# Optimization experiments

Measured on AMD Instinct MI355X. Metric: run time of the kernel, lower is better.

Reference implementation:

```python
import jax, jax.numpy as jnp
import numpy as np

# config constants
H = 2048          # hidden_size
I_MOE = 1408      # moe_intermediate_size
E = 8             # n_routed_experts
TOP_K = 2         # num_experts_per_tok
NG = 4            # n_group
TOPK_G = 2        # topk_group
SCALE = 2.5       # routed_scaling_factor
N_SHARED = 2      # n_shared_experts
I_SHARED = I_MOE * N_SHARED
B, S = 1, 2048


def setup_inputs() -> dict:
    key = jax.random.key(0)
    ks = jax.random.split(key, 9)
    sc = 0.02
    return {
        "x": jax.random.normal(ks[0], (B, S, H), dtype=jnp.float32),
        "router_weight": jax.random.normal(ks[1], (E, H), dtype=jnp.float32) * sc,
        "e_score_correction_bias": jnp.zeros((E,), dtype=jnp.float32),
        "gate_w": jax.random.normal(ks[2], (E, I_MOE, H), dtype=jnp.float32) * sc,
        "up_w": jax.random.normal(ks[3], (E, I_MOE, H), dtype=jnp.float32) * sc,
        "down_w": jax.random.normal(ks[4], (E, H, I_MOE), dtype=jnp.float32) * sc,
        "shared_gate_w": jax.random.normal(ks[5], (I_SHARED, H), dtype=jnp.float32) * sc,
        "shared_up_w": jax.random.normal(ks[6], (I_SHARED, H), dtype=jnp.float32) * sc,
        "shared_down_w": jax.random.normal(ks[7], (H, I_SHARED), dtype=jnp.float32) * sc,
    }


def _mlp(x, gw, uw, dw):
    # SwiGLU MLP: down( silu(gate(x)) * up(x) )
    return (jax.nn.silu(x @ gw.T) * (x @ uw.T)) @ dw.T


def _route(x2d, rw, bias):
    T = x2d.shape[0]
    logits = x2d.astype(jnp.float32) @ rw.astype(jnp.float32).T          # [T,E]
    scores = jax.nn.sigmoid(logits)                                       # [T,E]
    sfc = scores + bias[None, :]                                          # [T,E]
    # group scores: sum of top-2 per group
    grp = sfc.reshape(T, NG, E // NG)
    group_scores = jnp.sum(jax.lax.top_k(grp, 2)[0], axis=-1)             # [T,NG]
    grp_idx = jax.lax.top_k(group_scores, TOPK_G)[1]                      # [T,topk_group]
    group_mask = jnp.zeros((T, NG), jnp.float32).at[
        jnp.arange(T)[:, None], grp_idx].set(1.0)                         # [T,NG]
    score_mask = jnp.repeat(group_mask, E // NG, axis=1)                  # [T,E]
    masked = jnp.where(score_mask > 0, sfc, 0.0)
    topk_idx = jax.lax.top_k(masked, TOP_K)[1]                            # [T,K]
    topk_w = jnp.take_along_axis(scores, topk_idx, axis=1)                # [T,K]
    topk_w = topk_w / (jnp.sum(topk_w, axis=-1, keepdims=True) + 1e-20)   # norm_topk_prob
    return topk_idx, topk_w * SCALE


def reference(x, router_weight, e_score_correction_bias, gate_w, up_w, down_w,
              shared_gate_w, shared_up_w, shared_down_w):
    orig_shape = x.shape
    x2d = x.reshape(-1, H)                                                # [T,H]
    T = x2d.shape[0]
    topk_idx, topk_w = _route(x2d, router_weight, e_score_correction_bias)
    # per-token per-expert combine weights [T,E] (top-k indices are distinct per token)
    cw = jnp.zeros((T, E), jnp.float32).at[
        jnp.arange(T)[:, None], topk_idx].add(topk_w)

    def expert_body(acc, ws):
        gw, uw, dw, cwe = ws  # gw/uw:[I,H], dw:[H,I], cwe:[T]
        y = _mlp(x2d, gw, uw, dw)
        return acc + cwe[:, None] * y, None

    routed, _ = jax.lax.scan(expert_body, jnp.zeros_like(x2d),
                             (gate_w, up_w, down_w, cw.T))
    out = routed.reshape(orig_shape) + _mlp(x, shared_gate_w, shared_up_w, shared_down_w)
    return out
```

## Files before the change

kernel.cpp:

```cpp
#include <hip/hip_runtime.h>
#include <hip/hip_bf16.h>
#include <math.h>

#define H 2048
#define IMOE 1408
#define NEXP 8
#define T_TOK 2048
#define ISH 2816
#define SCALEF 2.5f

#define NT_GU_R (IMOE / 64)
#define NT_GU_S (ISH / 64)
#define NT_DN   (H / 128)
#define GU_GRID (39 * NT_GU_R + 16 * NT_GU_S)
#define DN_GRID (39 * NT_DN + 16 * NT_DN)

typedef __attribute__((ext_vector_type(8))) short short8;
typedef __attribute__((ext_vector_type(4))) short short4v;
typedef __attribute__((ext_vector_type(4))) float floatx4;

union U8 { short8 s; unsigned u[4]; };

__device__ inline float b2f(short v) {
    unsigned int u = ((unsigned int)(unsigned short)v) << 16;
    float f; __builtin_memcpy(&f, &u, 4); return f;
}
__device__ inline short f2b(float f) {
    __hip_bfloat16 h = __float2bfloat16(f);
    short s; __builtin_memcpy(&s, &h, 2); return s;
}
__device__ __forceinline__ unsigned pkbf16(float a, float b) {
    float2 t; t.x = a; t.y = b;
    __hip_bfloat162 h2 = __float22bfloat162_rn(t);
    unsigned u; __builtin_memcpy(&u, &h2, 4); return u;
}

__device__ __forceinline__ void async16(const short* g, short* l) {
    __builtin_amdgcn_global_load_lds(
        (const __attribute__((address_space(1))) unsigned*)g,
        (__attribute__((address_space(3))) unsigned*)l, 16, 0, 0);
}

__device__ __forceinline__ int xcd_map(int orig, int nwg) {
    int q = nwg >> 3, r = nwg & 7;
    int x = orig & 7, s = orig >> 3;
    int base = (x < r) ? x * (q + 1) : r * (q + 1) + (x - r) * q;
    return base + s;
}

__global__ __launch_bounds__(256) void router_kernel(
    const float* __restrict__ x, const float* __restrict__ rw,
    const float* __restrict__ bias,
    int* __restrict__ cnt, int* __restrict__ tokList, int* __restrict__ slotList,
    float* __restrict__ pairW)
{
    const int wid  = (blockIdx.x * 256 + threadIdx.x) >> 6;
    const int lane = threadIdx.x & 63;
    if (wid >= T_TOK) return;
    const float* xr = x + (size_t)wid * H;

    float acc[NEXP];
#pragma unroll
    for (int e = 0; e < NEXP; ++e) acc[e] = 0.f;

#pragma unroll
    for (int c = 0; c < 8; ++c) {
        int idx = (c * 64 + lane) * 4;
        floatx4 xv = *(const floatx4*)(xr + idx);
#pragma unroll
        for (int e = 0; e < NEXP; ++e) {
            floatx4 wv = *(const floatx4*)(rw + e * H + idx);
            acc[e] += xv.x * wv.x + xv.y * wv.y + xv.z * wv.z + xv.w * wv.w;
        }
    }
#pragma unroll
    for (int e = 0; e < NEXP; ++e)
        for (int off = 32; off; off >>= 1)
            acc[e] += __shfl_xor(acc[e], off, 64);

    if (lane == 0) {
        float s[NEXP], sfc[NEXP];
#pragma unroll
        for (int e = 0; e < NEXP; ++e) {
            s[e]   = 1.0f / (1.0f + expf(-acc[e]));
            sfc[e] = s[e] + bias[e];
        }
        float gs[4];
#pragma unroll
        for (int g = 0; g < 4; ++g) gs[g] = sfc[2 * g] + sfc[2 * g + 1];
        int g1 = 0;
        for (int g = 1; g < 4; ++g) if (gs[g] > gs[g1]) g1 = g;
        int g2 = -1;
        for (int g = 0; g < 4; ++g) {
            if (g == g1) continue;
            if (g2 < 0 || gs[g] > gs[g2]) g2 = g;
        }
        float msk[NEXP];
#pragma unroll
        for (int e = 0; e < NEXP; ++e) {
            int g = e >> 1;
            msk[e] = (g == g1 || g == g2) ? sfc[e] : 0.0f;
        }
        int e1 = 0;
        for (int e = 1; e < NEXP; ++e) if (msk[e] > msk[e1]) e1 = e;
        int e2 = -1;
        for (int e = 0; e < NEXP; ++e) {
            if (e == e1) continue;
            if (e2 < 0 || msk[e] > msk[e2]) e2 = e;
        }
        float w1 = s[e1], w2 = s[e2];
        float inv = SCALEF / (w1 + w2 + 1e-20f);
        w1 *= inv; w2 *= inv;
        int p1 = atomicAdd(&cnt[e1], 1);
        tokList[e1 * T_TOK + p1]  = wid;
        slotList[e1 * T_TOK + p1] = 2 * wid;
        pairW[2 * wid] = w1;
        int p2 = atomicAdd(&cnt[e2], 1);
        tokList[e2 * T_TOK + p2]  = wid;
        slotList[e2 * T_TOK + p2] = 2 * wid + 1;
        pairW[2 * wid + 1] = w2;
    }
}

__global__ void plan_kernel(const int* __restrict__ cnt, int* __restrict__ meta)
{
    if (blockIdx.x != 0 || threadIdx.x != 0) return;
    int base = 0, gu = 0, dn = 0;
    meta[20] = 0; meta[32] = 0;
    for (int e = 0; e < NEXP; ++e) {
        int M = cnt[e];
        meta[e] = M;
        meta[9 + e] = base;
        base += M;
        int MT = (M + 127) >> 7;
        gu += MT * NT_GU_R;
        dn += MT * NT_DN;
        meta[21 + e] = gu;
        meta[33 + e] = dn;
    }
    meta[8]  = T_TOK;
    meta[17] = 0;
    meta[29] = gu + 16 * NT_GU_S;
    meta[41] = dn + 16 * NT_DN;
}

__global__ __launch_bounds__(256) void convert_kernel(
    const float* __restrict__ src, short* __restrict__ dst, int n4)
{
    int idx = blockIdx.x * 256 + threadIdx.x;
    int stride = gridDim.x * 256;
    for (; idx < n4; idx += stride) {
        floatx4 v = *(const floatx4*)(src + (size_t)idx * 4);
        short4v o = { f2b(v.x), f2b(v.y), f2b(v.z), f2b(v.w) };
        *(short4v*)(dst + (size_t)idx * 4) = o;
    }
}

__global__ __launch_bounds__(256) void gu_gemm(
    const short* __restrict__ xb,
    const float* __restrict__ gw, const float* __restrict__ uw,
    const float* __restrict__ sgw, const float* __restrict__ suw,
    short* __restrict__ hiddenP, short* __restrict__ hiddenS,
    const int* __restrict__ tokList, const int* __restrict__ meta)
{
    const int total = meta[29];
    if (blockIdx.x >= total) return;
    const int idx = xcd_map(blockIdx.x, total);
    int e = 0;
    while (e < 8 && idx >= meta[21 + e]) ++e;

    int M, NT, Nout, rowBase;
    const float *b1, *b2;
    const int* gat;
    short* outP;
    if (e < 8) {
        M = meta[e]; NT = NT_GU_R; Nout = IMOE; rowBase = meta[9 + e];
        b1 = gw + (size_t)e * IMOE * H;
        b2 = uw + (size_t)e * IMOE * H;
        gat = tokList + e * T_TOK;
        outP = hiddenP;
    } else {
        M = T_TOK; NT = NT_GU_S; Nout = ISH; rowBase = 0;
        b1 = sgw; b2 = suw; gat = nullptr; outP = hiddenS;
    }
    const int MT = (M + 127) >> 7;
    const int local = idx - meta[20 + e];
    const int mt = local % MT;
    const int nt = local / MT;

    __shared__ short As[128 * 64];
    __shared__ short Bg[64 * 64];
    __shared__ short Bu[64 * 64];

    const int tid  = threadIdx.x;
    const int w    = tid >> 6;
    const int lane = tid & 63;
    const int quad = lane >> 4;
    const int l16  = lane & 15;
    const int wm = w >> 1, wn = w & 1;

    const int r8 = lane >> 3;
    const int cs = (lane & 7) ^ r8;
    const short* aSrc[4];
    short* ldsA[4];
#pragma unroll
    for (int i = 0; i < 4; ++i) {
        int r = w * 32 + i * 8 + r8;
        int p = mt * 128 + r;
        int pos = p < M ? p : (M - 1);
        int arow = gat ? gat[pos] : pos;
        aSrc[i] = xb + (size_t)arow * H + cs * 8;
        ldsA[i] = As + (w * 32 + i * 8) * 64;
    }

    const int br = tid >> 2;
    const int bj = tid & 3;
    const int bs = br & 7;
    const float* b1p = b1 + (size_t)(nt * 64 + br) * H + bj * 16;
    const float* b2p = b2 + (size_t)(nt * 64 + br) * H + bj * 16;
    short* bgDst0 = Bg + br * 64 + (((2 * bj)    ) ^ bs) * 8;
    short* bgDst1 = Bg + br * 64 + (((2 * bj) + 1) ^ bs) * 8;
    short* buDst0 = Bu + br * 64 + (((2 * bj)    ) ^ bs) * 8;
    short* buDst1 = Bu + br * 64 + (((2 * bj) + 1) ^ bs) * 8;

    floatx4 accg[4][2] = {};
    floatx4 accu[4][2] = {};

    for (int k0 = 0; k0 < H; k0 += 64) {
#pragma unroll
        for (int i = 0; i < 4; ++i)
            async16(aSrc[i] + k0, ldsA[i]);
        {
            floatx4 v0 = ((const floatx4*)(b1p + k0))[0];
            floatx4 v1 = ((const floatx4*)(b1p + k0))[1];
            floatx4 v2 = ((const floatx4*)(b1p + k0))[2];
            floatx4 v3 = ((const floatx4*)(b1p + k0))[3];
            U8 lo, hi;
            lo.u[0] = pkbf16(v0.x, v0.y); lo.u[1] = pkbf16(v0.z, v0.w);
            lo.u[2] = pkbf16(v1.x, v1.y); lo.u[3] = pkbf16(v1.z, v1.w);
            hi.u[0] = pkbf16(v2.x, v2.y); hi.u[1] = pkbf16(v2.z, v2.w);
            hi.u[2] = pkbf16(v3.x, v3.y); hi.u[3] = pkbf16(v3.z, v3.w);
            *(short8*)bgDst0 = lo.s;
            *(short8*)bgDst1 = hi.s;
        }
        {
            floatx4 v0 = ((const floatx4*)(b2p + k0))[0];
            floatx4 v1 = ((const floatx4*)(b2p + k0))[1];
            floatx4 v2 = ((const floatx4*)(b2p + k0))[2];
            floatx4 v3 = ((const floatx4*)(b2p + k0))[3];
            U8 lo, hi;
            lo.u[0] = pkbf16(v0.x, v0.y); lo.u[1] = pkbf16(v0.z, v0.w);
            lo.u[2] = pkbf16(v1.x, v1.y); lo.u[3] = pkbf16(v1.z, v1.w);
            hi.u[0] = pkbf16(v2.x, v2.y); hi.u[1] = pkbf16(v2.z, v2.w);
            hi.u[2] = pkbf16(v3.x, v3.y); hi.u[3] = pkbf16(v3.z, v3.w);
            *(short8*)buDst0 = lo.s;
            *(short8*)buDst1 = hi.s;
        }
        __syncthreads();
        const int sw = l16 & 7;
        short8 af[4], bgf[2], buf[2];
#pragma unroll
        for (int kk2 = 0; kk2 < 2; ++kk2) {
            const int c = kk2 * 4 + quad;
#pragma unroll
            for (int m = 0; m < 4; ++m)
                af[m] = *(const short8*)(As + (wm * 64 + m * 16 + l16) * 64 + (c ^ sw) * 8);
#pragma unroll
            for (int n = 0; n < 2; ++n) {
                bgf[n] = *(const short8*)(Bg + (wn * 32 + n * 16 + l16) * 64 + (c ^ sw) * 8);
                buf[n] = *(const short8*)(Bu + (wn * 32 + n * 16 + l16) * 64 + (c ^ sw) * 8);
            }
#pragma unroll
            for (int m = 0; m < 4; ++m)
#pragma unroll
                for (int n = 0; n < 2; ++n) {
                    accg[m][n] = __builtin_amdgcn_mfma_f32_16x16x32_bf16(af[m], bgf[n], accg[m][n], 0, 0, 0);
                    accu[m][n] = __builtin_amdgcn_mfma_f32_16x16x32_bf16(af[m], buf[n], accu[m][n], 0, 0, 0);
                }
        }
        __syncthreads();
    }

#pragma unroll
    for (int m = 0; m < 4; ++m) {
#pragma unroll
        for (int rr = 0; rr < 4; ++rr) {
            int lr = wm * 64 + m * 16 + quad * 4 + rr;
            int p = mt * 128 + lr;
            if (p >= M) continue;
            size_t rowoff = (size_t)(rowBase + p) * Nout + nt * 64 + wn * 32;
#pragma unroll
            for (int n = 0; n < 2; ++n) {
                float g = accg[m][n][rr];
                float u = accu[m][n][rr];
                outP[rowoff + n * 16 + l16] = f2b(g / (1.0f + __expf(-g)) * u);
            }
        }
    }
}

__global__ __launch_bounds__(256) void dn_gemm(
    const short* __restrict__ hiddenP, const short* __restrict__ hiddenS,
    const float* __restrict__ dw, const float* __restrict__ sdw,
    short* __restrict__ outPairs, short* __restrict__ sharedOut,
    const int* __restrict__ slotList, const int* __restrict__ meta)
{
    const int total = meta[41];
    if (blockIdx.x >= total) return;
    const int rtot = meta[40];
    int idx;
    if (blockIdx.x < rtot) idx = xcd_map(blockIdx.x, rtot);
    else                   idx = rtot + xcd_map(blockIdx.x - rtot, total - rtot);
    int e = 0;
    while (e < 8 && idx >= meta[33 + e]) ++e;

    int M, K, rowBase;
    const float* bp;
    const short* Abase;
    const int* scat;
    short* outP;
    if (e < 8) {
        M = meta[e]; K = IMOE; rowBase = meta[9 + e];
        bp = dw + (size_t)e * H * IMOE;
        Abase = hiddenP; scat = slotList + e * T_TOK; outP = outPairs;
    } else {
        M = T_TOK; K = ISH; rowBase = 0;
        bp = sdw; Abase = hiddenS; scat = nullptr; outP = sharedOut;
    }
    const int MT = (M + 127) >> 7;
    const int local = idx - meta[32 + e];
    const int mt = local % MT;
    const int nt = local / MT;

    __shared__ short As[128 * 64];
    __shared__ short Bs[128 * 64];

    const int tid  = threadIdx.x;
    const int w    = tid >> 6;
    const int lane = tid & 63;
    const int quad = lane >> 4;
    const int l16  = lane & 15;
    const int wm = w >> 1, wn = w & 1;

    const int r8 = lane >> 3;
    const int cs = (lane & 7) ^ r8;
    const short* aSrc[4];
    short* ldsA[4];
#pragma unroll
    for (int i = 0; i < 4; ++i) {
        int r = w * 32 + i * 8 + r8;
        int p = mt * 128 + r;
        int pos = p < M ? p : (M - 1);
        aSrc[i] = Abase + (size_t)(rowBase + pos) * K + cs * 8;
        ldsA[i] = As + (w * 32 + i * 8) * 64;
    }

    const int br = tid >> 1;
    const int bh = tid & 1;
    const int bs = br & 7;
    const float* bpp = bp + (size_t)(nt * 128 + br) * K + bh * 32;
    short* bDst[4];
#pragma unroll
    for (int i = 0; i < 4; ++i)
        bDst[i] = Bs + br * 64 + ((bh * 4 + i) ^ bs) * 8;

    floatx4 acc[4][4] = {};

    const int kIters = K >> 6;
    for (int kt = 0; kt < kIters; ++kt) {
        const int k0 = kt << 6;
#pragma unroll
        for (int i = 0; i < 4; ++i)
            async16(aSrc[i] + k0, ldsA[i]);
#pragma unroll
        for (int i = 0; i < 4; ++i) {
            floatx4 v0 = ((const floatx4*)(bpp + k0))[2 * i];
            floatx4 v1 = ((const floatx4*)(bpp + k0))[2 * i + 1];
            U8 c;
            c.u[0] = pkbf16(v0.x, v0.y); c.u[1] = pkbf16(v0.z, v0.w);
            c.u[2] = pkbf16(v1.x, v1.y); c.u[3] = pkbf16(v1.z, v1.w);
            *(short8*)bDst[i] = c.s;
        }
        __syncthreads();
        const int sw = l16 & 7;
        short8 af[4], bf[4];
#pragma unroll
        for (int kk2 = 0; kk2 < 2; ++kk2) {
            const int c = kk2 * 4 + quad;
#pragma unroll
            for (int m = 0; m < 4; ++m)
                af[m] = *(const short8*)(As + (wm * 64 + m * 16 + l16) * 64 + (c ^ sw) * 8);
#pragma unroll
            for (int n = 0; n < 4; ++n)
                bf[n] = *(const short8*)(Bs + (wn * 64 + n * 16 + l16) * 64 + (c ^ sw) * 8);
#pragma unroll
            for (int m = 0; m < 4; ++m)
#pragma unroll
                for (int n = 0; n < 4; ++n)
                    acc[m][n] = __builtin_amdgcn_mfma_f32_16x16x32_bf16(af[m], bf[n], acc[m][n], 0, 0, 0);
        }
        __syncthreads();
    }

#pragma unroll
    for (int m = 0; m < 4; ++m) {
#pragma unroll
        for (int rr = 0; rr < 4; ++rr) {
            int lr = wm * 64 + m * 16 + quad * 4 + rr;
            int p = mt * 128 + lr;
            if (p >= M) continue;
            int crow = scat ? scat[p] : p;
            size_t rowoff = (size_t)crow * H + nt * 128 + wn * 64;
#pragma unroll
            for (int n = 0; n < 4; ++n)
                outP[rowoff + n * 16 + l16] = f2b(acc[m][n][rr]);
        }
    }
}

__global__ __launch_bounds__(256) void combine_kernel(
    const short* __restrict__ outPairs, const short* __restrict__ sharedOut,
    const float* __restrict__ pairW, float* __restrict__ out)
{
    size_t gi = ((size_t)blockIdx.x * 256 + threadIdx.x) * 8;
    int t = (int)(gi >> 11);
    int h = (int)(gi & (H - 1));
    float w0 = pairW[2 * t], w1 = pairW[2 * t + 1];
    short8 p0 = *(const short8*)(outPairs + (size_t)(2 * t) * H + h);
    short8 p1 = *(const short8*)(outPairs + (size_t)(2 * t + 1) * H + h);
    short8 sh = *(const short8*)(sharedOut + gi);
    floatx4 o0, o1;
#pragma unroll
    for (int j = 0; j < 4; ++j)
        o0[j] = w0 * b2f(p0[j]) + w1 * b2f(p1[j]) + b2f(sh[j]);
#pragma unroll
    for (int j = 0; j < 4; ++j)
        o1[j] = w0 * b2f(p0[4 + j]) + w1 * b2f(p1[4 + j]) + b2f(sh[4 + j]);
    *(floatx4*)(out + gi)     = o0;
    *(floatx4*)(out + gi + 4) = o1;
}

extern "C" void kernel_launch(void* const* d_in, const int* in_sizes, int n_in,
                              void* d_out, int out_size, void* d_ws, size_t ws_size,
                              hipStream_t stream)
{
    const float* x    = (const float*)d_in[0];
    const float* rw   = (const float*)d_in[1];
    const float* bias = (const float*)d_in[2];
    const float* gw   = (const float*)d_in[3];
    const float* uw   = (const float*)d_in[4];
    const float* dw   = (const float*)d_in[5];
    const float* sgw  = (const float*)d_in[6];
    const float* suw  = (const float*)d_in[7];
    const float* sdw  = (const float*)d_in[8];
    float* out = (float*)d_out;

    char* ws = (char*)d_ws;
    size_t off = 0;
    auto alloc = [&](size_t bytes) {
        off = (off + 255) & ~(size_t)255;
        void* p = ws + off;
        off += bytes;
        return p;
    };
    int*   cnt       = (int*)  alloc(NEXP * sizeof(int));
    int*   tokList   = (int*)  alloc((size_t)NEXP * T_TOK * sizeof(int));
    int*   slotList  = (int*)  alloc((size_t)NEXP * T_TOK * sizeof(int));
    float* pairW     = (float*)alloc((size_t)2 * T_TOK * sizeof(float));
    int*   meta      = (int*)  alloc(64 * sizeof(int));
    short* xb        = (short*)alloc((size_t)T_TOK * H * sizeof(short));
    short* hiddenP   = (short*)alloc((size_t)2 * T_TOK * IMOE * sizeof(short));
    short* hiddenS   = (short*)alloc((size_t)T_TOK * ISH * sizeof(short));
    short* outPairs  = (short*)alloc((size_t)2 * T_TOK * H * sizeof(short));
    short* sharedOut = (short*)alloc((size_t)T_TOK * H * sizeof(short));
    (void)ws_size;

    hipMemsetAsync(cnt, 0, NEXP * sizeof(int), stream);

    router_kernel<<<T_TOK / 4, 256, 0, stream>>>(x, rw, bias, cnt, tokList, slotList, pairW);
    plan_kernel<<<1, 64, 0, stream>>>(cnt, meta);
    convert_kernel<<<2048, 256, 0, stream>>>(x, xb, T_TOK * H / 4);

    gu_gemm<<<GU_GRID, 256, 0, stream>>>(xb, gw, uw, sgw, suw,
                                         hiddenP, hiddenS, tokList, meta);
    dn_gemm<<<DN_GRID, 256, 0, stream>>>(hiddenP, hiddenS, dw, sdw,
                                         outPairs, sharedOut, slotList, meta);

    combine_kernel<<<(T_TOK * H / 8) / 256, 256, 0, stream>>>(outPairs, sharedOut, pairW, out);
}
```

Baseline: 687.5 us.

## Pre-convert all weights to bf16 in a separate pass and async-load into LDS

Adds a kernel that converts all expert and shared weights from fp32 to bf16 into workspace buffers each call. The gate/up and down GEMMs then stage weight tiles with direct global-to-LDS async loads instead of loading fp32 into registers and packing to bf16 in the main loop. This removes conversion ALU work and register staging from the GEMM inner loop and halves weight bytes per tile reread. It adds a full extra read/write pass over all weights per call.

```diff
diff --git a/kernel.cpp b/kernel.cpp
--- a/kernel.cpp
+++ b/kernel.cpp
@@ -19,8 +19,6 @@
 typedef __attribute__((ext_vector_type(4))) short short4v;
 typedef __attribute__((ext_vector_type(4))) float floatx4;
 
-union U8 { short8 s; unsigned u[4]; };
-
 __device__ inline float b2f(short v) {
     unsigned int u = ((unsigned int)(unsigned short)v) << 16;
     float f; __builtin_memcpy(&f, &u, 4); return f;
@@ -28,11 +26,6 @@
 __device__ inline short f2b(float f) {
     __hip_bfloat16 h = __float2bfloat16(f);
     short s; __builtin_memcpy(&s, &h, 2); return s;
-}
-__device__ __forceinline__ unsigned pkbf16(float a, float b) {
-    float2 t; t.x = a; t.y = b;
-    __hip_bfloat162 h2 = __float22bfloat162_rn(t);
-    unsigned u; __builtin_memcpy(&u, &h2, 4); return u;
 }
 
 __device__ __forceinline__ void async16(const short* g, short* l) {
@@ -156,10 +149,46 @@
     }
 }
 
+#define W8_GU  2883584
+#define W8_SH  720896
+#define W8_S1  (W8_GU)
+#define W8_S2  (2*W8_GU)
+#define W8_S3  (3*W8_GU)
+#define W8_S4  (3*W8_GU + W8_SH)
+#define W8_S5  (3*W8_GU + 2*W8_SH)
+#define W8_S6  (3*W8_GU + 3*W8_SH)
+__global__ __launch_bounds__(256) void wconvert_kernel(
+    const float* __restrict__ gw, const float* __restrict__ uw,
+    const float* __restrict__ dw, const float* __restrict__ sgw,
+    const float* __restrict__ suw, const float* __restrict__ sdw,
+    short* __restrict__ gwb, short* __restrict__ uwb, short* __restrict__ dwb,
+    short* __restrict__ sgwb, short* __restrict__ suwb, short* __restrict__ sdwb)
+{
+    int idx = blockIdx.x * 256 + threadIdx.x;
+    int stride = gridDim.x * 256;
+    for (; idx < W8_S6; idx += stride) {
+        const float* s; short* d; int local;
+        if (idx < W8_S3) {
+            if (idx < W8_S1)      { s = gw;  d = gwb;  local = idx; }
+            else if (idx < W8_S2) { s = uw;  d = uwb;  local = idx - W8_S1; }
+            else                  { s = dw;  d = dwb;  local = idx - W8_S2; }
+        } else {
+            if (idx < W8_S4)      { s = sgw; d = sgwb; local = idx - W8_S3; }
+            else if (idx < W8_S5) { s = suw; d = suwb; local = idx - W8_S4; }
+            else                  { s = sdw; d = sdwb; local = idx - W8_S5; }
+        }
+        floatx4 v0 = *(const floatx4*)(s + (size_t)local * 8);
+        floatx4 v1 = *(const floatx4*)(s + (size_t)local * 8 + 4);
+        short8 o = { f2b(v0.x), f2b(v0.y), f2b(v0.z), f2b(v0.w),
+                     f2b(v1.x), f2b(v1.y), f2b(v1.z), f2b(v1.w) };
+        *(short8*)(d + (size_t)local * 8) = o;
+    }
+}
+
 __global__ __launch_bounds__(256) void gu_gemm(
     const short* __restrict__ xb,
-    const float* __restrict__ gw, const float* __restrict__ uw,
-    const float* __restrict__ sgw, const float* __restrict__ suw,
+    const short* __restrict__ gwb, const short* __restrict__ uwb,
+    const short* __restrict__ sgwb, const short* __restrict__ suwb,
     short* __restrict__ hiddenP, short* __restrict__ hiddenS,
     const int* __restrict__ tokList, const int* __restrict__ meta)
 {
@@ -170,18 +199,18 @@
     while (e < 8 && idx >= meta[21 + e]) ++e;
 
     int M, NT, Nout, rowBase;
-    const float *b1, *b2;
+    const short *b1, *b2;
     const int* gat;
     short* outP;
     if (e < 8) {
         M = meta[e]; NT = NT_GU_R; Nout = IMOE; rowBase = meta[9 + e];
-        b1 = gw + (size_t)e * IMOE * H;
-        b2 = uw + (size_t)e * IMOE * H;
+        b1 = gwb + (size_t)e * IMOE * H;
+        b2 = uwb + (size_t)e * IMOE * H;
         gat = tokList + e * T_TOK;
         outP = hiddenP;
     } else {
         M = T_TOK; NT = NT_GU_S; Nout = ISH; rowBase = 0;
-        b1 = sgw; b2 = suw; gat = nullptr; outP = hiddenS;
+        b1 = sgwb; b2 = suwb; gat = nullptr; outP = hiddenS;
     }
     const int MT = (M + 127) >> 7;
     const int local = idx - meta[20 + e];
@@ -189,8 +218,7 @@
     const int nt = local / MT;
 
     __shared__ short As[128 * 64];
-    __shared__ short Bg[64 * 64];
-    __shared__ short Bu[64 * 64];
+    __shared__ short Bgu[128 * 64];
 
     const int tid  = threadIdx.x;
     const int w    = tid >> 6;
@@ -202,7 +230,9 @@
     const int r8 = lane >> 3;
     const int cs = (lane & 7) ^ r8;
     const short* aSrc[4];
+    const short* bSrc[4];
     short* ldsA[4];
+    short* ldsB[4];
 #pragma unroll
     for (int i = 0; i < 4; ++i) {
         int r = w * 32 + i * 8 + r8;
@@ -211,51 +241,20 @@
         int arow = gat ? gat[pos] : pos;
         aSrc[i] = xb + (size_t)arow * H + cs * 8;
         ldsA[i] = As + (w * 32 + i * 8) * 64;
-    }
-
-    const int br = tid >> 2;
-    const int bj = tid & 3;
-    const int bs = br & 7;
-    const float* b1p = b1 + (size_t)(nt * 64 + br) * H + bj * 16;
-    const float* b2p = b2 + (size_t)(nt * 64 + br) * H + bj * 16;
-    short* bgDst0 = Bg + br * 64 + (((2 * bj)    ) ^ bs) * 8;
-    short* bgDst1 = Bg + br * 64 + (((2 * bj) + 1) ^ bs) * 8;
-    short* buDst0 = Bu + br * 64 + (((2 * bj)    ) ^ bs) * 8;
-    short* buDst1 = Bu + br * 64 + (((2 * bj) + 1) ^ bs) * 8;
+        const short* wsrc = (r < 64) ? (b1 + (size_t)(nt * 64 + r) * H)
+                                     : (b2 + (size_t)(nt * 64 + r - 64) * H);
+        bSrc[i] = wsrc + cs * 8;
+        ldsB[i] = Bgu + (w * 32 + i * 8) * 64;
+    }
 
     floatx4 accg[4][2] = {};
     floatx4 accu[4][2] = {};
 
     for (int k0 = 0; k0 < H; k0 += 64) {
 #pragma unroll
-        for (int i = 0; i < 4; ++i)
-            async16(aSrc[i] + k0, ldsA[i]);
-        {
-            floatx4 v0 = ((const floatx4*)(b1p + k0))[0];
-            floatx4 v1 = ((const floatx4*)(b1p + k0))[1];
-            floatx4 v2 = ((const floatx4*)(b1p + k0))[2];
-            floatx4 v3 = ((const floatx4*)(b1p + k0))[3];
-            U8 lo, hi;
-            lo.u[0] = pkbf16(v0.x, v0.y); lo.u[1] = pkbf16(v0.z, v0.w);
-            lo.u[2] = pkbf16(v1.x, v1.y); lo.u[3] = pkbf16(v1.z, v1.w);
-            hi.u[0] = pkbf16(v2.x, v2.y); hi.u[1] = pkbf16(v2.z, v2.w);
-            hi.u[2] = pkbf16(v3.x, v3.y); hi.u[3] = pkbf16(v3.z, v3.w);
-            *(short8*)bgDst0 = lo.s;
-            *(short8*)bgDst1 = hi.s;
-        }
-        {
-            floatx4 v0 = ((const floatx4*)(b2p + k0))[0];
-            floatx4 v1 = ((const floatx4*)(b2p + k0))[1];
-            floatx4 v2 = ((const floatx4*)(b2p + k0))[2];
-            floatx4 v3 = ((const floatx4*)(b2p + k0))[3];
-            U8 lo, hi;
-            lo.u[0] = pkbf16(v0.x, v0.y); lo.u[1] = pkbf16(v0.z, v0.w);
-            lo.u[2] = pkbf16(v1.x, v1.y); lo.u[3] = pkbf16(v1.z, v1.w);
-            hi.u[0] = pkbf16(v2.x, v2.y); hi.u[1] = pkbf16(v2.z, v2.w);
-            hi.u[2] = pkbf16(v3.x, v3.y); hi.u[3] = pkbf16(v3.z, v3.w);
-            *(short8*)buDst0 = lo.s;
-            *(short8*)buDst1 = hi.s;
-        }
+        for (int i = 0; i < 4; ++i) async16(aSrc[i] + k0, ldsA[i]);
+#pragma unroll
+        for (int i = 0; i < 4; ++i) async16(bSrc[i] + k0, ldsB[i]);
         __syncthreads();
         const int sw = l16 & 7;
         short8 af[4], bgf[2], buf[2];
@@ -267,8 +266,8 @@
                 af[m] = *(const short8*)(As + (wm * 64 + m * 16 + l16) * 64 + (c ^ sw) * 8);
 #pragma unroll
             for (int n = 0; n < 2; ++n) {
-                bgf[n] = *(const short8*)(Bg + (wn * 32 + n * 16 + l16) * 64 + (c ^ sw) * 8);
-                buf[n] = *(const short8*)(Bu + (wn * 32 + n * 16 + l16) * 64 + (c ^ sw) * 8);
+                bgf[n] = *(const short8*)(Bgu + (wn * 32 + n * 16 + l16) * 64 + (c ^ sw) * 8);
+                buf[n] = *(const short8*)(Bgu + (64 + wn * 32 + n * 16 + l16) * 64 + (c ^ sw) * 8);
             }
 #pragma unroll
             for (int m = 0; m < 4; ++m)
@@ -301,7 +300,7 @@
 
 __global__ __launch_bounds__(256) void dn_gemm(
     const short* __restrict__ hiddenP, const short* __restrict__ hiddenS,
-    const float* __restrict__ dw, const float* __restrict__ sdw,
+    const short* __restrict__ dwb, const short* __restrict__ sdwb,
     short* __restrict__ outPairs, short* __restrict__ sharedOut,
     const int* __restrict__ slotList, const int* __restrict__ meta)
 {
@@ -315,17 +314,17 @@
     while (e < 8 && idx >= meta[33 + e]) ++e;
 
     int M, K, rowBase;
-    const float* bp;
+    const short* bp;
     const short* Abase;
     const int* scat;
     short* outP;
     if (e < 8) {
         M = meta[e]; K = IMOE; rowBase = meta[9 + e];
-        bp = dw + (size_t)e * H * IMOE;
+        bp = dwb + (size_t)e * H * IMOE;
         Abase = hiddenP; scat = slotList + e * T_TOK; outP = outPairs;
     } else {
         M = T_TOK; K = ISH; rowBase = 0;
-        bp = sdw; Abase = hiddenS; scat = nullptr; outP = sharedOut;
+        bp = sdwb; Abase = hiddenS; scat = nullptr; outP = sharedOut;
     }
     const int MT = (M + 127) >> 7;
     const int local = idx - meta[32 + e];
@@ -345,7 +344,9 @@
     const int r8 = lane >> 3;
     const int cs = (lane & 7) ^ r8;
     const short* aSrc[4];
+    const short* bSrc[4];
     short* ldsA[4];
+    short* ldsB[4];
 #pragma unroll
     for (int i = 0; i < 4; ++i) {
         int r = w * 32 + i * 8 + r8;
@@ -353,16 +354,9 @@
         int pos = p < M ? p : (M - 1);
         aSrc[i] = Abase + (size_t)(rowBase + pos) * K + cs * 8;
         ldsA[i] = As + (w * 32 + i * 8) * 64;
-    }
-
-    const int br = tid >> 1;
-    const int bh = tid & 1;
-    const int bs = br & 7;
-    const float* bpp = bp + (size_t)(nt * 128 + br) * K + bh * 32;
-    short* bDst[4];
-#pragma unroll
-    for (int i = 0; i < 4; ++i)
-        bDst[i] = Bs + br * 64 + ((bh * 4 + i) ^ bs) * 8;
+        bSrc[i] = bp + (size_t)(nt * 128 + r) * K + cs * 8;
+        ldsB[i] = Bs + (w * 32 + i * 8) * 64;
+    }
 
     floatx4 acc[4][4] = {};
 
@@ -370,17 +364,9 @@
     for (int kt = 0; kt < kIters; ++kt) {
         const int k0 = kt << 6;
 #pragma unroll
-        for (int i = 0; i < 4; ++i)
-            async16(aSrc[i] + k0, ldsA[i]);
-#pragma unroll
-        for (int i = 0; i < 4; ++i) {
-            floatx4 v0 = ((const floatx4*)(bpp + k0))[2 * i];
-            floatx4 v1 = ((const floatx4*)(bpp + k0))[2 * i + 1];
-            U8 c;
-            c.u[0] = pkbf16(v0.x, v0.y); c.u[1] = pkbf16(v0.z, v0.w);
-            c.u[2] = pkbf16(v1.x, v1.y); c.u[3] = pkbf16(v1.z, v1.w);
-            *(short8*)bDst[i] = c.s;
-        }
+        for (int i = 0; i < 4; ++i) async16(aSrc[i] + k0, ldsA[i]);
+#pragma unroll
+        for (int i = 0; i < 4; ++i) async16(bSrc[i] + k0, ldsB[i]);
         __syncthreads();
         const int sw = l16 & 7;
         short8 af[4], bf[4];
@@ -473,6 +459,12 @@
     short* hiddenS   = (short*)alloc((size_t)T_TOK * ISH * sizeof(short));
     short* outPairs  = (short*)alloc((size_t)2 * T_TOK * H * sizeof(short));
     short* sharedOut = (short*)alloc((size_t)T_TOK * H * sizeof(short));
+    short* gwb  = (short*)alloc((size_t)NEXP * IMOE * H * sizeof(short));
+    short* uwb  = (short*)alloc((size_t)NEXP * IMOE * H * sizeof(short));
+    short* dwb  = (short*)alloc((size_t)NEXP * H * IMOE * sizeof(short));
+    short* sgwb = (short*)alloc((size_t)ISH * H * sizeof(short));
+    short* suwb = (short*)alloc((size_t)ISH * H * sizeof(short));
+    short* sdwb = (short*)alloc((size_t)H * ISH * sizeof(short));
     (void)ws_size;
 
     hipMemsetAsync(cnt, 0, NEXP * sizeof(int), stream);
@@ -480,10 +472,12 @@
     router_kernel<<<T_TOK / 4, 256, 0, stream>>>(x, rw, bias, cnt, tokList, slotList, pairW);
     plan_kernel<<<1, 64, 0, stream>>>(cnt, meta);
     convert_kernel<<<2048, 256, 0, stream>>>(x, xb, T_TOK * H / 4);
-
-    gu_gemm<<<GU_GRID, 256, 0, stream>>>(xb, gw, uw, sgw, suw,
+    wconvert_kernel<<<2048, 256, 0, stream>>>(gw, uw, dw, sgw, suw, sdw,
+                                              gwb, uwb, dwb, sgwb, suwb, sdwb);
+
+    gu_gemm<<<GU_GRID, 256, 0, stream>>>(xb, gwb, uwb, sgwb, suwb,
                                          hiddenP, hiddenS, tokList, meta);
-    dn_gemm<<<DN_GRID, 256, 0, stream>>>(hiddenP, hiddenS, dw, sdw,
+    dn_gemm<<<DN_GRID, 256, 0, stream>>>(hiddenP, hiddenS, dwb, sdwb,
                                          outPairs, sharedOut, slotList, meta);
 
     combine_kernel<<<(T_TOK * H / 8) / 256, 256, 0, stream>>>(outPairs, sharedOut, pairW, out);
```

New measurement: 657.6 us. 1.05x faster.

## Stage fp32 weights to LDS asynchronously and fuse x conversion into router

Applied to the files above, without the earlier changes.

Both GEMM kernels now load fp32 weight tiles straight into LDS with global_load_lds, using an XOR swizzle. The bf16 packing moves to after the LDS read, inside the MFMA fragment load, instead of passing through registers during staging. The separate fp32-to-bf16 conversion kernel for x is removed and folded into the router kernel, which already reads x. This doubles LDS footprint for the B tiles, which may lower occupancy, and every wave now repeats the conversion work after each LDS read.

```diff
diff --git a/kernel.cpp b/kernel.cpp
--- a/kernel.cpp
+++ b/kernel.cpp
@@ -40,6 +40,11 @@
         (const __attribute__((address_space(1))) unsigned*)g,
         (__attribute__((address_space(3))) unsigned*)l, 16, 0, 0);
 }
+__device__ __forceinline__ void async16f(const float* g, float* l) {
+    __builtin_amdgcn_global_load_lds(
+        (const __attribute__((address_space(1))) unsigned*)g,
+        (__attribute__((address_space(3))) unsigned*)l, 16, 0, 0);
+}
 
 __device__ __forceinline__ int xcd_map(int orig, int nwg) {
     int q = nwg >> 3, r = nwg & 7;
@@ -52,12 +57,13 @@
     const float* __restrict__ x, const float* __restrict__ rw,
     const float* __restrict__ bias,
     int* __restrict__ cnt, int* __restrict__ tokList, int* __restrict__ slotList,
-    float* __restrict__ pairW)
+    float* __restrict__ pairW, short* __restrict__ xb)
 {
     const int wid  = (blockIdx.x * 256 + threadIdx.x) >> 6;
     const int lane = threadIdx.x & 63;
     if (wid >= T_TOK) return;
     const float* xr = x + (size_t)wid * H;
+    short* xbrow = xb + (size_t)wid * H;
 
     float acc[NEXP];
 #pragma unroll
@@ -72,6 +78,8 @@
             floatx4 wv = *(const floatx4*)(rw + e * H + idx);
             acc[e] += xv.x * wv.x + xv.y * wv.y + xv.z * wv.z + xv.w * wv.w;
         }
+        short4v o = { f2b(xv.x), f2b(xv.y), f2b(xv.z), f2b(xv.w) };
+        *(short4v*)(xbrow + idx) = o;
     }
 #pragma unroll
     for (int e = 0; e < NEXP; ++e)
@@ -144,18 +152,6 @@
     meta[41] = dn + 16 * NT_DN;
 }
 
-__global__ __launch_bounds__(256) void convert_kernel(
-    const float* __restrict__ src, short* __restrict__ dst, int n4)
-{
-    int idx = blockIdx.x * 256 + threadIdx.x;
-    int stride = gridDim.x * 256;
-    for (; idx < n4; idx += stride) {
-        floatx4 v = *(const floatx4*)(src + (size_t)idx * 4);
-        short4v o = { f2b(v.x), f2b(v.y), f2b(v.z), f2b(v.w) };
-        *(short4v*)(dst + (size_t)idx * 4) = o;
-    }
-}
-
 __global__ __launch_bounds__(256) void gu_gemm(
     const short* __restrict__ xb,
     const float* __restrict__ gw, const float* __restrict__ uw,
@@ -189,8 +185,8 @@
     const int nt = local / MT;
 
     __shared__ short As[128 * 64];
-    __shared__ short Bg[64 * 64];
-    __shared__ short Bu[64 * 64];
+    __shared__ float Bg[64 * 64];
+    __shared__ float Bu[64 * 64];
 
     const int tid  = threadIdx.x;
     const int w    = tid >> 6;
@@ -200,7 +196,7 @@
     const int wm = w >> 1, wn = w & 1;
 
     const int r8 = lane >> 3;
-    const int cs = (lane & 7) ^ r8;
+    const int csA = (lane & 7) ^ r8;
     const short* aSrc[4];
     short* ldsA[4];
 #pragma unroll
@@ -209,54 +205,39 @@
         int p = mt * 128 + r;
         int pos = p < M ? p : (M - 1);
         int arow = gat ? gat[pos] : pos;
-        aSrc[i] = xb + (size_t)arow * H + cs * 8;
+        aSrc[i] = xb + (size_t)arow * H + csA * 8;
         ldsA[i] = As + (w * 32 + i * 8) * 64;
     }
 
-    const int br = tid >> 2;
-    const int bj = tid & 3;
-    const int bs = br & 7;
-    const float* b1p = b1 + (size_t)(nt * 64 + br) * H + bj * 16;
-    const float* b2p = b2 + (size_t)(nt * 64 + br) * H + bj * 16;
-    short* bgDst0 = Bg + br * 64 + (((2 * bj)    ) ^ bs) * 8;
-    short* bgDst1 = Bg + br * 64 + (((2 * bj) + 1) ^ bs) * 8;
-    short* buDst0 = Bu + br * 64 + (((2 * bj)    ) ^ bs) * 8;
-    short* buDst1 = Bu + br * 64 + (((2 * bj) + 1) ^ bs) * 8;
+    const int br4 = lane >> 4;
+    const int bc  = lane & 15;
+    const float* bgSrc[4];
+    const float* buSrc[4];
+    float* ldsBg[4];
+    float* ldsBu[4];
+#pragma unroll
+    for (int i = 0; i < 4; ++i) {
+        int rb = w * 16 + i * 4;
+        int row = rb + br4;
+        int sc = bc ^ (row & 15);
+        bgSrc[i] = b1 + (size_t)(nt * 64 + row) * H + sc * 4;
+        buSrc[i] = b2 + (size_t)(nt * 64 + row) * H + sc * 4;
+        ldsBg[i] = Bg + rb * 64;
+        ldsBu[i] = Bu + rb * 64;
+    }
 
     floatx4 accg[4][2] = {};
     floatx4 accu[4][2] = {};
 
     for (int k0 = 0; k0 < H; k0 += 64) {
 #pragma unroll
-        for (int i = 0; i < 4; ++i)
-            async16(aSrc[i] + k0, ldsA[i]);
-        {
-            floatx4 v0 = ((const floatx4*)(b1p + k0))[0];
-            floatx4 v1 = ((const floatx4*)(b1p + k0))[1];
-            floatx4 v2 = ((const floatx4*)(b1p + k0))[2];
-            floatx4 v3 = ((const floatx4*)(b1p + k0))[3];
-            U8 lo, hi;
-            lo.u[0] = pkbf16(v0.x, v0.y); lo.u[1] = pkbf16(v0.z, v0.w);
-            lo.u[2] = pkbf16(v1.x, v1.y); lo.u[3] = pkbf16(v1.z, v1.w);
-            hi.u[0] = pkbf16(v2.x, v2.y); hi.u[1] = pkbf16(v2.z, v2.w);
-            hi.u[2] = pkbf16(v3.x, v3.y); hi.u[3] = pkbf16(v3.z, v3.w);
-            *(short8*)bgDst0 = lo.s;
-            *(short8*)bgDst1 = hi.s;
-        }
-        {
-            floatx4 v0 = ((const floatx4*)(b2p + k0))[0];
-            floatx4 v1 = ((const floatx4*)(b2p + k0))[1];
-            floatx4 v2 = ((const floatx4*)(b2p + k0))[2];
-            floatx4 v3 = ((const floatx4*)(b2p + k0))[3];
-            U8 lo, hi;
-            lo.u[0] = pkbf16(v0.x, v0.y); lo.u[1] = pkbf16(v0.z, v0.w);
-            lo.u[2] = pkbf16(v1.x, v1.y); lo.u[3] = pkbf16(v1.z, v1.w);
-            hi.u[0] = pkbf16(v2.x, v2.y); hi.u[1] = pkbf16(v2.z, v2.w);
-            hi.u[2] = pkbf16(v3.x, v3.y); hi.u[3] = pkbf16(v3.z, v3.w);
-            *(short8*)buDst0 = lo.s;
-            *(short8*)buDst1 = hi.s;
-        }
+        for (int i = 0; i < 4; ++i) async16(aSrc[i] + k0, ldsA[i]);
+#pragma unroll
+        for (int i = 0; i < 4; ++i) async16f(bgSrc[i] + k0, ldsBg[i]);
+#pragma unroll
+        for (int i = 0; i < 4; ++i) async16f(buSrc[i] + k0, ldsBu[i]);
         __syncthreads();
+
         const int sw = l16 & 7;
         short8 af[4], bgf[2], buf[2];
 #pragma unroll
@@ -267,8 +248,22 @@
                 af[m] = *(const short8*)(As + (wm * 64 + m * 16 + l16) * 64 + (c ^ sw) * 8);
 #pragma unroll
             for (int n = 0; n < 2; ++n) {
-                bgf[n] = *(const short8*)(Bg + (wn * 32 + n * 16 + l16) * 64 + (c ^ sw) * 8);
-                buf[n] = *(const short8*)(Bu + (wn * 32 + n * 16 + l16) * 64 + (c ^ sw) * 8);
+                int rg = wn * 32 + n * 16 + l16;
+                const float* pg = Bg + rg * 64;
+                const float* pu = Bu + rg * 64;
+                int j0 = ((2 * c)     ^ (rg & 15)) * 4;
+                int j1 = ((2 * c + 1) ^ (rg & 15)) * 4;
+                floatx4 g0 = *(const floatx4*)(pg + j0);
+                floatx4 g1 = *(const floatx4*)(pg + j1);
+                floatx4 u0 = *(const floatx4*)(pu + j0);
+                floatx4 u1 = *(const floatx4*)(pu + j1);
+                U8 tg, tu;
+                tg.u[0] = pkbf16(g0.x, g0.y); tg.u[1] = pkbf16(g0.z, g0.w);
+                tg.u[2] = pkbf16(g1.x, g1.y); tg.u[3] = pkbf16(g1.z, g1.w);
+                tu.u[0] = pkbf16(u0.x, u0.y); tu.u[1] = pkbf16(u0.z, u0.w);
+                tu.u[2] = pkbf16(u1.x, u1.y); tu.u[3] = pkbf16(u1.z, u1.w);
+                bgf[n] = tg.s;
+                buf[n] = tu.s;
             }
 #pragma unroll
             for (int m = 0; m < 4; ++m)
@@ -333,7 +328,7 @@
     const int nt = local / MT;
 
     __shared__ short As[128 * 64];
-    __shared__ short Bs[128 * 64];
+    __shared__ float Bf[128 * 64];
 
     const int tid  = threadIdx.x;
     const int w    = tid >> 6;
@@ -343,7 +338,7 @@
     const int wm = w >> 1, wn = w & 1;
 
     const int r8 = lane >> 3;
-    const int cs = (lane & 7) ^ r8;
+    const int csA = (lane & 7) ^ r8;
     const short* aSrc[4];
     short* ldsA[4];
 #pragma unroll
@@ -351,18 +346,22 @@
         int r = w * 32 + i * 8 + r8;
         int p = mt * 128 + r;
         int pos = p < M ? p : (M - 1);
-        aSrc[i] = Abase + (size_t)(rowBase + pos) * K + cs * 8;
+        aSrc[i] = Abase + (size_t)(rowBase + pos) * K + csA * 8;
         ldsA[i] = As + (w * 32 + i * 8) * 64;
     }
 
-    const int br = tid >> 1;
-    const int bh = tid & 1;
-    const int bs = br & 7;
-    const float* bpp = bp + (size_t)(nt * 128 + br) * K + bh * 32;
-    short* bDst[4];
-#pragma unroll
-    for (int i = 0; i < 4; ++i)
-        bDst[i] = Bs + br * 64 + ((bh * 4 + i) ^ bs) * 8;
+    const int br4 = lane >> 4;
+    const int bc  = lane & 15;
+    const float* bSrc[8];
+    float* ldsB[8];
+#pragma unroll
+    for (int i = 0; i < 8; ++i) {
+        int rb = w * 32 + i * 4;
+        int row = rb + br4;
+        int sc = bc ^ (row & 15);
+        bSrc[i] = bp + (size_t)(nt * 128 + row) * K + sc * 4;
+        ldsB[i] = Bf + rb * 64;
+    }
 
     floatx4 acc[4][4] = {};
 
@@ -370,18 +369,11 @@
     for (int kt = 0; kt < kIters; ++kt) {
         const int k0 = kt << 6;
 #pragma unroll
-        for (int i = 0; i < 4; ++i)
-            async16(aSrc[i] + k0, ldsA[i]);
-#pragma unroll
-        for (int i = 0; i < 4; ++i) {
-            floatx4 v0 = ((const floatx4*)(bpp + k0))[2 * i];
-            floatx4 v1 = ((const floatx4*)(bpp + k0))[2 * i + 1];
-            U8 c;
-            c.u[0] = pkbf16(v0.x, v0.y); c.u[1] = pkbf16(v0.z, v0.w);
-            c.u[2] = pkbf16(v1.x, v1.y); c.u[3] = pkbf16(v1.z, v1.w);
-            *(short8*)bDst[i] = c.s;
-        }
+        for (int i = 0; i < 4; ++i) async16(aSrc[i] + k0, ldsA[i]);
+#pragma unroll
+        for (int i = 0; i < 8; ++i) async16f(bSrc[i] + k0, ldsB[i]);
         __syncthreads();
+
         const int sw = l16 & 7;
         short8 af[4], bf[4];
 #pragma unroll
@@ -391,8 +383,16 @@
             for (int m = 0; m < 4; ++m)
                 af[m] = *(const short8*)(As + (wm * 64 + m * 16 + l16) * 64 + (c ^ sw) * 8);
 #pragma unroll
-            for (int n = 0; n < 4; ++n)
-                bf[n] = *(const short8*)(Bs + (wn * 64 + n * 16 + l16) * 64 + (c ^ sw) * 8);
+            for (int n = 0; n < 4; ++n) {
+                int rb2 = wn * 64 + n * 16 + l16;
+                const float* pb = Bf + rb2 * 64;
+                floatx4 b0 = *(const floatx4*)(pb + (((2 * c)     ^ (rb2 & 15)) * 4));
+                floatx4 b1 = *(const floatx4*)(pb + (((2 * c + 1) ^ (rb2 & 15)) * 4));
+                U8 t;
+                t.u[0] = pkbf16(b0.x, b0.y); t.u[1] = pkbf16(b0.z, b0.w);
+                t.u[2] = pkbf16(b1.x, b1.y); t.u[3] = pkbf16(b1.z, b1.w);
+                bf[n] = t.s;
+            }
 #pragma unroll
             for (int m = 0; m < 4; ++m)
 #pragma unroll
@@ -477,9 +477,8 @@
 
     hipMemsetAsync(cnt, 0, NEXP * sizeof(int), stream);
 
-    router_kernel<<<T_TOK / 4, 256, 0, stream>>>(x, rw, bias, cnt, tokList, slotList, pairW);
+    router_kernel<<<T_TOK / 4, 256, 0, stream>>>(x, rw, bias, cnt, tokList, slotList, pairW, xb);
     plan_kernel<<<1, 64, 0, stream>>>(cnt, meta);
-    convert_kernel<<<2048, 256, 0, stream>>>(x, xb, T_TOK * H / 4);
 
     gu_gemm<<<GU_GRID, 256, 0, stream>>>(xb, gw, uw, sgw, suw,
                                          hiddenP, hiddenS, tokList, meta);
```

Measured after the change: 622.9 us. 9.4% less time.
